# Optimization experiments

Measured on AMD Instinct MI355X. Metric: run time of the kernel, lower is better.

## Reference

```python
import jax, jax.numpy as jnp
import numpy as np

# Contiguous token segment lengths per group (static, sums to 4096)
LEN_GROUPS = (256, 512, 768, 384, 640, 512, 576, 448)
NUM_GROUPS, D_IN, D_OUT = 8, 512, 512
BATCH = 16


def setup_inputs() -> dict:
    key = jax.random.key(0)
    k1, k2, k3 = jax.random.split(key, 3)
    T = int(sum(LEN_GROUPS))
    x = jax.random.normal(k1, (BATCH, T, D_IN), dtype=jnp.float32)
    # nn.Linear default init: U(-1/sqrt(fan_in), 1/sqrt(fan_in))
    bound = 1.0 / np.sqrt(D_IN)
    W = jax.random.uniform(k2, (NUM_GROUPS, D_OUT, D_IN), jnp.float32, -bound, bound)
    b = jax.random.uniform(k3, (NUM_GROUPS, D_OUT), jnp.float32, -bound, bound)
    return {"x": x, "W": W, "b": b}


def reference(x, W, b):
    # Per-group Linear over contiguous token segments, then concat along tokens.
    # Loop is over a small static group count; segment bounds are Python ints,
    # so slicing is static and jit-compatible.
    outs = []
    start = 0
    for i, L in enumerate(LEN_GROUPS):
        seg = x[:, start:start + L]                     # [B, L, D_in]
        outs.append(jnp.einsum('btd,od->bto', seg, W[i]) + b[i])  # [B, L, D_out]
        start += L
    return jnp.concatenate(outs, axis=1)               # [B, T, D_out]
```

## Files before the change

### kernel.cpp

```cpp
#include <hip/hip_runtime.h>
#include <hip/hip_bf16.h>
#include <cstdint>

#define BATCH 16
#define TTOT  4096
#define DIN   512
#define DOUT  512
#define NG    8
#define NJOB  33

typedef float f32x4 __attribute__((ext_vector_type(4)));
typedef short s16x8 __attribute__((ext_vector_type(8)));

__device__ __forceinline__ short f2b(float f) {
    union { __bf16 b; short s; } u; u.b = (__bf16)f; return u.s;
}

__device__ __constant__ short JT0[NJOB] = {
    0,128, 256,384,512,640, 768,896,1024,1152,1280,1408, 1536,1664,1792,
    1920,2048,2176,2304,2432, 2560,2688,2816,2944, 3072,3200,3328,3456,
    3584, 3648, 3712,3840,3968};
__device__ __constant__ char JG[NJOB] = {
    0,0, 1,1,1,1, 2,2,2,2,2,2, 3,3,3, 4,4,4,4,4, 5,5,5,5, 6,6,6,6, 6, 7, 7,7,7};
__device__ __constant__ char JNW[NJOB] = {
    8,8, 8,8,8,8, 8,8,8,8,8,8, 8,8,8, 8,8,8,8,8, 8,8,8,8, 8,8,8,8, 4, 4, 8,8,8};

__global__ void wconv_kernel(const float* __restrict__ W, ushort* __restrict__ wbf) {
    int gid = blockIdx.x * 256 + threadIdx.x;
    int c = gid >> 10;
    int q = (gid & 1023) << 4;
    int row = q >> 7;
    int bc  = q & 127;
    int kbyte = bc ^ ((row & 7) << 4);
    int kt = c & 7, nt = (c >> 3) & 3, g = c >> 5;
    const float* wp = W + ((size_t)(g * DOUT + nt * 128 + row)) * DIN
                        + kt * 64 + (kbyte >> 1);
    float4 v0 = *reinterpret_cast<const float4*>(wp);
    float4 v1 = *reinterpret_cast<const float4*>(wp + 4);
    s16x8 o;
    o[0]=f2b(v0.x); o[1]=f2b(v0.y); o[2]=f2b(v0.z); o[3]=f2b(v0.w);
    o[4]=f2b(v1.x); o[5]=f2b(v1.y); o[6]=f2b(v1.z); o[7]=f2b(v1.w);
    *reinterpret_cast<s16x8*>((char*)wbf + (size_t)c * 16384 + q) = o;
}

__launch_bounds__(512, 2)
__global__ void gemm_kernel(const float* __restrict__ x,
                            const ushort* __restrict__ wbf,
                            const float* __restrict__ bias,
                            float* __restrict__ out) {
    __shared__ __align__(16) char smem[147968];
    char* ldsB = smem;
    const int tid  = threadIdx.x;
    const int lane = tid & 63;
    const int wv   = tid >> 6;
    const int colf = lane & 15;
    const int kg   = lane >> 4;
    float* cslice = (float*)(smem + 131072 + wv * 2112);

    const int p  = blockIdx.x;
    const int l  = ((p & 7) << 5) + (p >> 3);
    const int r0   = (l < 64) ? l * 9 : 8 * l + 64;
    const int rend = r0 + ((l < 64) ? 9 : 8);

    float4 st0[4], st1[4], st2[4], st3[4];

#define ISSUE(S, P, KT_) do {                                               \
        const float* p_ = (P) + ((KT_) << 6) + (kg << 3);                   \
        st##S[0] = *(const float4*)(p_);                                    \
        st##S[1] = *(const float4*)(p_ + 4);                                \
        st##S[2] = *(const float4*)(p_ + 32);                               \
        st##S[3] = *(const float4*)(p_ + 36);                               \
    } while (0)

#define CONSUME(S, KT_) do {                                                \
        _Pragma("unroll")                                                   \
        for (int ks = 0; ks < 2; ++ks) {                                    \
            float4 f0 = st##S[ks*2], f1 = st##S[ks*2+1];                    \
            s16x8 af;                                                       \
            af[0]=f2b(f0.x); af[1]=f2b(f0.y); af[2]=f2b(f0.z); af[3]=f2b(f0.w); \
            af[4]=f2b(f1.x); af[5]=f2b(f1.y); af[6]=f2b(f1.z); af[7]=f2b(f1.w); \
            const int kb = ks * 64 + (kg << 4);                             \
            _Pragma("unroll")                                               \
            for (int ni = 0; ni < 8; ++ni) {                                \
                int rb = ni * 16 + colf;                                    \
                s16x8 bf = *(const s16x8*)(ldsB + (KT_) * 16384 + (rb << 7) \
                                           + (kb ^ ((rb & 7) << 4)));       \
                acc[ni] = __builtin_amdgcn_mfma_f32_16x16x32_bf16(          \
                    af, bf, acc[ni], 0, 0, 0);                              \
            }                                                               \
        }                                                                   \
    } while (0)

#define FENCE asm volatile("" ::: "memory")

    auto abase = [&](int r) -> const float* {
        int job = r >> 6, bb = r & 15;
        return x + ((size_t)(bb * TTOT + (int)JT0[job] + (wv << 4) + colf)) * DIN;
    };

    const float* pcur = abase(r0);
    ISSUE(0, pcur, 0); ISSUE(1, pcur, 1); ISSUE(2, pcur, 2);

    int key_cur = -1;
#pragma unroll 1
    for (int r = r0; r < rend; ++r) {
        const int job = r >> 6, nt = (r >> 4) & 3, bb = r & 15;
        const int t0 = JT0[job], g = JG[job], nw = JNW[job];
        const int key = (g << 2) | nt;
        if (key != key_cur) {
            key_cur = key;
            FENCE;
            __builtin_amdgcn_s_barrier();
            FENCE;
            const char* wsrc = (const char*)wbf + (size_t)key * 131072;
#pragma unroll
            for (int i = 0; i < 16; ++i) {
                __builtin_amdgcn_global_load_lds(
                    (const __attribute__((address_space(1))) void*)(wsrc + i * 8192 + tid * 16),
                    (__attribute__((address_space(3))) void*)(ldsB + i * 8192 + tid * 16),
                    16, 0, 0);
            }
            FENCE;
            asm volatile("s_waitcnt vmcnt(0)" ::: "memory");
            __builtin_amdgcn_s_barrier();
            FENCE;
        }
        const bool hn = (r + 1 < rend);
        const float* pnext = hn ? abase(r + 1) : pcur;

        f32x4 acc[8];
#pragma unroll
        for (int ni = 0; ni < 8; ++ni) acc[ni] = (f32x4){0.f, 0.f, 0.f, 0.f};

        ISSUE(3, pcur, 3);            CONSUME(0, 0);
        ISSUE(0, pcur, 4);            CONSUME(1, 1);
        ISSUE(1, pcur, 5);            CONSUME(2, 2);
        ISSUE(2, pcur, 6);            CONSUME(3, 3);
        ISSUE(3, pcur, 7);            CONSUME(0, 4);
        if (hn) { ISSUE(0, pnext, 0); } CONSUME(1, 5);
        if (hn) { ISSUE(1, pnext, 1); } CONSUME(2, 6);
        if (hn) { ISSUE(2, pnext, 2); } CONSUME(3, 7);

        if (wv < nw) {
            const int n0 = nt << 7;
            const float4 b0 = *(const float4*)(bias + (g << 9) + n0 + (colf << 2));
            const float4 b1 = *(const float4*)(bias + (g << 9) + n0 + (colf << 2) + 64);
            const size_t orow0 = (size_t)bb * TTOT + t0 + (wv << 4);
#pragma unroll
            for (int j = 0; j < 4; ++j) {
#pragma unroll
                for (int ni = 0; ni < 8; ++ni)
                    cslice[kg * 132 + ni * 16 + colf] = acc[ni][j];
                float4 v0 = *(const float4*)(cslice + kg * 132 + (colf << 2));
                float4 v1 = *(const float4*)(cslice + kg * 132 + (colf << 2) + 64);
                float4 o0, o1;
                o0.x = v0.x + b0.x; o0.y = v0.y + b0.y;
                o0.z = v0.z + b0.z; o0.w = v0.w + b0.w;
                o1.x = v1.x + b1.x; o1.y = v1.y + b1.y;
                o1.z = v1.z + b1.z; o1.w = v1.w + b1.w;
                float* orow = out + (orow0 + (kg << 2) + j) * DOUT + n0;
                *(float4*)(orow + (colf << 2))      = o0;
                *(float4*)(orow + (colf << 2) + 64) = o1;
            }
        }
        pcur = pnext;
    }
#undef ISSUE
#undef CONSUME
#undef FENCE
}

__launch_bounds__(256)
__global__ void gemm_fallback(const float* __restrict__ x,
                              const float* __restrict__ W,
                              const float* __restrict__ bias,
                              float* __restrict__ out) {
    __shared__ __align__(16) char smem[49152];
    const int tid  = threadIdx.x;
    const int lane = tid & 63;
    const int wid  = tid >> 6;
    const int wm   = wid >> 1;
    const int wn   = wid & 1;
    const int p  = blockIdx.x;
    const int l  = ((p & 7) << 9) + (p >> 3);
    const int mt = l >> 2;
    const int nt = l & 3;
    const int bb = mt >> 6;
    const int t0 = (mt & 63) << 6;
    const int n0 = nt << 7;
    int g = 0;
    if (t0 >= 256)  g++; if (t0 >= 768)  g++; if (t0 >= 1536) g++;
    if (t0 >= 1920) g++; if (t0 >= 2560) g++; if (t0 >= 3072) g++;
    if (t0 >= 3648) g++;
    const int arow = tid >> 2;
    const int acol = (tid & 3) << 4;
    const float* aptr = x + ((size_t)(bb * TTOT + t0 + arow)) * DIN + acol;
    float4 a0, a1, a2, a3;
    float4 bw0[4], bw1[4];
    auto load_global = [&](int k0) {
        a0 = *(const float4*)(aptr + k0);
        a1 = *(const float4*)(aptr + k0 + 4);
        a2 = *(const float4*)(aptr + k0 + 8);
        a3 = *(const float4*)(aptr + k0 + 12);
#pragma unroll
        for (int pp = 0; pp < 4; ++pp) {
            int idx = pp * 256 + tid;
            int row = idx >> 3, seg = idx & 7;
            const float* wp = W + ((size_t)((g << 9) + n0 + row)) * DIN + k0 + (seg << 3);
            bw0[pp] = *(const float4*)(wp);
            bw1[pp] = *(const float4*)(wp + 4);
        }
    };
    auto swz = [](int row, int bc) { return (row << 7) + (bc ^ ((row & 7) << 4)); };
    auto write_lds = [&](int buf) {
        char* ab  = smem + buf * 8192;
        char* bb_ = smem + 16384 + buf * 16384;
        s16x8 w0, w1;
        w0[0]=f2b(a0.x); w0[1]=f2b(a0.y); w0[2]=f2b(a0.z); w0[3]=f2b(a0.w);
        w0[4]=f2b(a1.x); w0[5]=f2b(a1.y); w0[6]=f2b(a1.z); w0[7]=f2b(a1.w);
        w1[0]=f2b(a2.x); w1[1]=f2b(a2.y); w1[2]=f2b(a2.z); w1[3]=f2b(a2.w);
        w1[4]=f2b(a3.x); w1[5]=f2b(a3.y); w1[6]=f2b(a3.z); w1[7]=f2b(a3.w);
        const int abase2 = acol << 1;
        *(s16x8*)(ab + swz(arow, abase2))      = w0;
        *(s16x8*)(ab + swz(arow, abase2 + 16)) = w1;
#pragma unroll
        for (int pp = 0; pp < 4; ++pp) {
            int idx = pp * 256 + tid;
            int row = idx >> 3, seg = idx & 7;
            s16x8 wvv;
            wvv[0]=f2b(bw0[pp].x); wvv[1]=f2b(bw0[pp].y);
            wvv[2]=f2b(bw0[pp].z); wvv[3]=f2b(bw0[pp].w);
            wvv[4]=f2b(bw1[pp].x); wvv[5]=f2b(bw1[pp].y);
            wvv[6]=f2b(bw1[pp].z); wvv[7]=f2b(bw1[pp].w);
            *(s16x8*)(bb_ + swz(row, seg << 4)) = wvv;
        }
    };
    f32x4 acc[2][4];
#pragma unroll
    for (int mi = 0; mi < 2; ++mi)
#pragma unroll
        for (int ni = 0; ni < 4; ++ni) acc[mi][ni] = (f32x4){0.f,0.f,0.f,0.f};
    const int colf = lane & 15;
    const int kgrp = lane >> 4;
    auto compute = [&](int buf) {
        const char* ab  = smem + buf * 8192;
        const char* bb_ = smem + 16384 + buf * 16384;
#pragma unroll
        for (int ks = 0; ks < 2; ++ks) {
            const int kb = ks * 64 + kgrp * 16;
            s16x8 af[2], bf[4];
#pragma unroll
            for (int mi = 0; mi < 2; ++mi)
                af[mi] = *(const s16x8*)(ab + swz(wm * 32 + mi * 16 + colf, kb));
#pragma unroll
            for (int ni = 0; ni < 4; ++ni)
                bf[ni] = *(const s16x8*)(bb_ + swz(wn * 64 + ni * 16 + colf, kb));
#pragma unroll
            for (int mi = 0; mi < 2; ++mi)
#pragma unroll
                for (int ni = 0; ni < 4; ++ni)
                    acc[mi][ni] = __builtin_amdgcn_mfma_f32_16x16x32_bf16(
                        af[mi], bf[ni], acc[mi][ni], 0, 0, 0);
        }
    };
    load_global(0);
    write_lds(0);
    __syncthreads();
    int buf = 0;
#pragma unroll 1
    for (int kt = 0; kt < 8; ++kt) {
        if (kt < 7) load_global((kt + 1) << 6);
        compute(buf);
        if (kt < 7) write_lds(buf ^ 1);
        __syncthreads();
        buf ^= 1;
    }
    float* cbuf = (float*)smem;
#pragma unroll
    for (int ni = 0; ni < 4; ++ni) {
        const int c = wn * 64 + ni * 16 + colf;
#pragma unroll
        for (int mi = 0; mi < 2; ++mi) {
            const int r = wm * 32 + mi * 16 + kgrp * 4;
            f32x4 v = acc[mi][ni];
            cbuf[(r + 0) * 132 + c] = v[0];
            cbuf[(r + 1) * 132 + c] = v[1];
            cbuf[(r + 2) * 132 + c] = v[2];
            cbuf[(r + 3) * 132 + c] = v[3];
        }
    }
    __syncthreads();
    const int rr = tid >> 5;
    const int cc = (tid & 31) << 2;
    const float4 bv = *(const float4*)(bias + (g << 9) + n0 + cc);
#pragma unroll
    for (int it = 0; it < 8; ++it) {
        const int row = it * 8 + rr;
        float4 v = *(const float4*)(cbuf + row * 132 + cc);
        float4 o4; o4.x = v.x + bv.x; o4.y = v.y + bv.y;
                   o4.z = v.z + bv.z; o4.w = v.w + bv.w;
        *(float4*)(out + ((size_t)(bb * TTOT) + t0 + row) * DOUT + n0 + cc) = o4;
    }
}

extern "C" void kernel_launch(void* const* d_in, const int* in_sizes, int n_in,
                              void* d_out, int out_size, void* d_ws, size_t ws_size,
                              hipStream_t stream) {
    const float* x    = (const float*)d_in[0];
    const float* W    = (const float*)d_in[1];
    const float* bias = (const float*)d_in[2];
    float* out = (float*)d_out;

    const size_t wbytes = (size_t)NG * DOUT * DIN * sizeof(ushort);

    if (ws_size >= wbytes) {
        ushort* wbf = (ushort*)d_ws;
        wconv_kernel<<<1024, 256, 0, stream>>>(W, wbf);
        gemm_kernel<<<256, 512, 0, stream>>>(x, wbf, bias, out);
    } else {
        gemm_fallback<<<BATCH * 64 * 4, 256, 0, stream>>>(x, W, bias, out);
    }
}
```

Baseline: 105.7 us.

## Restructure grouped GEMM into 64-column N-chunks with flattened batch-token tiles

The GEMM is redone so each block owns one 64-column output chunk of one group, keeping a 64 KB bf16 weight slice resident in LDS that is loaded once. Each block walks flattened (batch, token) rows, using magic-number division to map them back to batch and token. This replaces the per-job weight reloads and barriers, as well as the LDS-staged output transpose. The grid doubles to 512 blocks with occupancy 4, and the rows are register-prefetched two k-steps ahead. A risk is that x rows are now re-read eight times across N-chunks (versus four before), and output stores become scalar instead of float4.

```diff
diff --git a/kernel.cpp b/kernel.cpp
--- a/kernel.cpp
+++ b/kernel.cpp
@@ -7,7 +7,6 @@
 #define DIN   512
 #define DOUT  512
 #define NG    8
-#define NJOB  33
 
 typedef float f32x4 __attribute__((ext_vector_type(4)));
 typedef short s16x8 __attribute__((ext_vector_type(8)));
@@ -16,158 +15,177 @@
     union { __bf16 b; short s; } u; u.b = (__bf16)f; return u.s;
 }
 
-__device__ __constant__ short JT0[NJOB] = {
-    0,128, 256,384,512,640, 768,896,1024,1152,1280,1408, 1536,1664,1792,
-    1920,2048,2176,2304,2432, 2560,2688,2816,2944, 3072,3200,3328,3456,
-    3584, 3648, 3712,3840,3968};
-__device__ __constant__ char JG[NJOB] = {
-    0,0, 1,1,1,1, 2,2,2,2,2,2, 3,3,3, 4,4,4,4,4, 5,5,5,5, 6,6,6,6, 6, 7, 7,7,7};
-__device__ __constant__ char JNW[NJOB] = {
-    8,8, 8,8,8,8, 8,8,8,8,8,8, 8,8,8, 8,8,8,8,8, 8,8,8,8, 8,8,8,8, 4, 4, 8,8,8};
+__device__ __constant__ short GT0[8] = {0,256,768,1536,1920,2560,3072,3648};
+__device__ __constant__ short GL[8]  = {256,512,768,384,640,512,576,448};
+__device__ __constant__ int   GM[8]  = {16385,8193,5462,10923,6554,8193,7282,9363};
+__device__ __constant__ char PG[64] = {
+    0,0,0,0,
+    1,1,1,1,1,1,1,1,
+    2,2,2,2,2,2,2,2,2,2,2,2,
+    3,3,3,3,3,3,
+    4,4,4,4,4,4,4,4,4,4,
+    5,5,5,5,5,5,5,5,
+    6,6,6,6,6,6,6,6,6,
+    7,7,7,7,7,7,7};
+__device__ __constant__ char PS[64] = {
+    0,1,2,3,
+    0,1,2,3,4,5,6,7,
+    0,1,2,3,4,5,6,7,8,9,10,11,
+    0,1,2,3,4,5,
+    0,1,2,3,4,5,6,7,8,9,
+    0,1,2,3,4,5,6,7,
+    0,1,2,3,4,5,6,7,8,
+    0,1,2,3,4,5,6};
 
 __global__ void wconv_kernel(const float* __restrict__ W, ushort* __restrict__ wbf) {
     int gid = blockIdx.x * 256 + threadIdx.x;
-    int c = gid >> 10;
-    int q = (gid & 1023) << 4;
+    int c = gid >> 9;
+    int q = (gid & 511) << 4;
     int row = q >> 7;
     int bc  = q & 127;
     int kbyte = bc ^ ((row & 7) << 4);
-    int kt = c & 7, nt = (c >> 3) & 3, g = c >> 5;
-    const float* wp = W + ((size_t)(g * DOUT + nt * 128 + row)) * DIN
-                        + kt * 64 + (kbyte >> 1);
+    int kt = c & 7, nc = (c >> 3) & 7, g = c >> 6;
+    const float* wp = W + ((size_t)((g << 9) + (nc << 6) + row) << 9)
+                        + (kt << 6) + (kbyte >> 1);
     float4 v0 = *reinterpret_cast<const float4*>(wp);
     float4 v1 = *reinterpret_cast<const float4*>(wp + 4);
     s16x8 o;
     o[0]=f2b(v0.x); o[1]=f2b(v0.y); o[2]=f2b(v0.z); o[3]=f2b(v0.w);
     o[4]=f2b(v1.x); o[5]=f2b(v1.y); o[6]=f2b(v1.z); o[7]=f2b(v1.w);
-    *reinterpret_cast<s16x8*>((char*)wbf + (size_t)c * 16384 + q) = o;
-}
-
-__launch_bounds__(512, 2)
+    *reinterpret_cast<s16x8*>((char*)wbf + (size_t)c * 8192 + q) = o;
+}
+
+__launch_bounds__(512, 4)
 __global__ void gemm_kernel(const float* __restrict__ x,
                             const ushort* __restrict__ wbf,
                             const float* __restrict__ bias,
                             float* __restrict__ out) {
-    __shared__ __align__(16) char smem[147968];
-    char* ldsB = smem;
+    __shared__ __align__(16) char ldsB[65536];
+
     const int tid  = threadIdx.x;
     const int lane = tid & 63;
     const int wv   = tid >> 6;
     const int colf = lane & 15;
     const int kg   = lane >> 4;
-    float* cslice = (float*)(smem + 131072 + wv * 2112);
-
-    const int p  = blockIdx.x;
-    const int l  = ((p & 7) << 5) + (p >> 3);
-    const int r0   = (l < 64) ? l * 9 : 8 * l + 64;
-    const int rend = r0 + ((l < 64) ? 9 : 8);
-
-    float4 st0[4], st1[4], st2[4], st3[4];
-
-#define ISSUE(S, P, KT_) do {                                               \
-        const float* p_ = (P) + ((KT_) << 6) + (kg << 3);                   \
-        st##S[0] = *(const float4*)(p_);                                    \
-        st##S[1] = *(const float4*)(p_ + 4);                                \
-        st##S[2] = *(const float4*)(p_ + 32);                               \
-        st##S[3] = *(const float4*)(p_ + 36);                               \
+
+    const int p    = blockIdx.x;
+    const int nc   = (p >> 3) & 7;
+    const int pair = (p & 7) + ((p >> 6) << 3);
+    const int g    = PG[pair];
+    const int s    = PS[pair];
+    const int t0g  = GT0[g];
+    const int Lg   = GL[g];
+    const int Mg   = GM[g];
+
+    const char* wsrc = (const char*)wbf + (size_t)((g << 3) + nc) * 65536;
+#pragma unroll
+    for (int i = 0; i < 8; ++i)
+        __builtin_amdgcn_global_load_lds(
+            (const __attribute__((address_space(1))) void*)(wsrc + i * 8192 + tid * 16),
+            (__attribute__((address_space(3))) void*)(ldsB + i * 8192 + tid * 16),
+            16, 0, 0);
+    asm volatile("s_waitcnt vmcnt(0)" ::: "memory");
+    __builtin_amdgcn_s_barrier();
+
+    float bv[4];
+#pragma unroll
+    for (int ni = 0; ni < 4; ++ni)
+        bv[ni] = bias[(g << 9) + (nc << 6) + (ni << 4) + colf];
+
+    const int swz = (colf & 7) << 4;
+    int bcoA[4], bcoB[4];
+#pragma unroll
+    for (int ni = 0; ni < 4; ++ni) {
+        int base = (((ni << 4) + colf) << 7) + ((kg << 4) ^ swz);
+        bcoA[ni] = base;
+        bcoB[ni] = base ^ 64;
+    }
+
+    const int fbase = s << 10;
+
+    auto aptr = [&](int f) -> const float* {
+        int bb = ((f >> 6) * Mg) >> 16;
+        int tt = f - bb * Lg;
+        return x + ((size_t)((bb << 12) + t0g + tt) << 9) + (kg << 3);
+    };
+
+    float4 sA[2][2][2];
+    const float *a0, *a1, *na0, *na1;
+
+#define LD(SL, KS) do {                                        \
+        sA[SL][0][0] = *(const float4*)(a0 + (KS) * 32);       \
+        sA[SL][0][1] = *(const float4*)(a0 + (KS) * 32 + 4);   \
+        sA[SL][1][0] = *(const float4*)(a1 + (KS) * 32);       \
+        sA[SL][1][1] = *(const float4*)(a1 + (KS) * 32 + 4);   \
     } while (0)
 
-#define CONSUME(S, KT_) do {                                                \
-        _Pragma("unroll")                                                   \
-        for (int ks = 0; ks < 2; ++ks) {                                    \
-            float4 f0 = st##S[ks*2], f1 = st##S[ks*2+1];                    \
-            s16x8 af;                                                       \
-            af[0]=f2b(f0.x); af[1]=f2b(f0.y); af[2]=f2b(f0.z); af[3]=f2b(f0.w); \
-            af[4]=f2b(f1.x); af[5]=f2b(f1.y); af[6]=f2b(f1.z); af[7]=f2b(f1.w); \
-            const int kb = ks * 64 + (kg << 4);                             \
-            _Pragma("unroll")                                               \
-            for (int ni = 0; ni < 8; ++ni) {                                \
-                int rb = ni * 16 + colf;                                    \
-                s16x8 bf = *(const s16x8*)(ldsB + (KT_) * 16384 + (rb << 7) \
-                                           + (kb ^ ((rb & 7) << 4)));       \
-                acc[ni] = __builtin_amdgcn_mfma_f32_16x16x32_bf16(          \
-                    af, bf, acc[ni], 0, 0, 0);                              \
-            }                                                               \
-        }                                                                   \
-    } while (0)
-
-#define FENCE asm volatile("" ::: "memory")
-
-    auto abase = [&](int r) -> const float* {
-        int job = r >> 6, bb = r & 15;
-        return x + ((size_t)(bb * TTOT + (int)JT0[job] + (wv << 4) + colf)) * DIN;
-    };
-
-    const float* pcur = abase(r0);
-    ISSUE(0, pcur, 0); ISSUE(1, pcur, 1); ISSUE(2, pcur, 2);
-
-    int key_cur = -1;
+    {
+        int f0 = fbase + (wv << 5);
+        a0 = aptr(f0 + colf);
+        a1 = aptr(f0 + 16 + colf);
+    }
+    LD(0, 0);
+    LD(1, 1);
+
 #pragma unroll 1
-    for (int r = r0; r < rend; ++r) {
-        const int job = r >> 6, nt = (r >> 4) & 3, bb = r & 15;
-        const int t0 = JT0[job], g = JG[job], nw = JNW[job];
-        const int key = (g << 2) | nt;
-        if (key != key_cur) {
-            key_cur = key;
-            FENCE;
-            __builtin_amdgcn_s_barrier();
-            FENCE;
-            const char* wsrc = (const char*)wbf + (size_t)key * 131072;
-#pragma unroll
-            for (int i = 0; i < 16; ++i) {
-                __builtin_amdgcn_global_load_lds(
-                    (const __attribute__((address_space(1))) void*)(wsrc + i * 8192 + tid * 16),
-                    (__attribute__((address_space(3))) void*)(ldsB + i * 8192 + tid * 16),
-                    16, 0, 0);
+    for (int t = 0; t < 4; ++t) {
+        f32x4 acc[2][4];
+#pragma unroll
+        for (int mi = 0; mi < 2; ++mi)
+#pragma unroll
+            for (int ni = 0; ni < 4; ++ni)
+                acc[mi][ni] = (f32x4){0.f, 0.f, 0.f, 0.f};
+
+#pragma unroll
+        for (int ks = 0; ks < 16; ++ks) {
+            s16x8 af[2];
+#pragma unroll
+            for (int mi = 0; mi < 2; ++mi) {
+                float4 lo = sA[ks & 1][mi][0], hi = sA[ks & 1][mi][1];
+                s16x8 o;
+                o[0]=f2b(lo.x); o[1]=f2b(lo.y); o[2]=f2b(lo.z); o[3]=f2b(lo.w);
+                o[4]=f2b(hi.x); o[5]=f2b(hi.y); o[6]=f2b(hi.z); o[7]=f2b(hi.w);
+                af[mi] = o;
             }
-            FENCE;
-            asm volatile("s_waitcnt vmcnt(0)" ::: "memory");
-            __builtin_amdgcn_s_barrier();
-            FENCE;
-        }
-        const bool hn = (r + 1 < rend);
-        const float* pnext = hn ? abase(r + 1) : pcur;
-
-        f32x4 acc[8];
-#pragma unroll
-        for (int ni = 0; ni < 8; ++ni) acc[ni] = (f32x4){0.f, 0.f, 0.f, 0.f};
-
-        ISSUE(3, pcur, 3);            CONSUME(0, 0);
-        ISSUE(0, pcur, 4);            CONSUME(1, 1);
-        ISSUE(1, pcur, 5);            CONSUME(2, 2);
-        ISSUE(2, pcur, 6);            CONSUME(3, 3);
-        ISSUE(3, pcur, 7);            CONSUME(0, 4);
-        if (hn) { ISSUE(0, pnext, 0); } CONSUME(1, 5);
-        if (hn) { ISSUE(1, pnext, 1); } CONSUME(2, 6);
-        if (hn) { ISSUE(2, pnext, 2); } CONSUME(3, 7);
-
-        if (wv < nw) {
-            const int n0 = nt << 7;
-            const float4 b0 = *(const float4*)(bias + (g << 9) + n0 + (colf << 2));
-            const float4 b1 = *(const float4*)(bias + (g << 9) + n0 + (colf << 2) + 64);
-            const size_t orow0 = (size_t)bb * TTOT + t0 + (wv << 4);
+            if (ks == 13 && t < 3) {
+                int f0n = fbase + ((((t + 1) << 3) + wv) << 5);
+                na0 = aptr(f0n + colf);
+                na1 = aptr(f0n + 16 + colf);
+            }
+            if (ks <= 13) {
+                LD(ks & 1, ks + 2);
+            } else if (t < 3) {
+                if (ks == 14) { a0 = na0; a1 = na1; LD(0, 0); }
+                else          { LD(1, 1); }
+            }
+            const char* bsl = ldsB + ((ks >> 1) << 13);
+            s16x8 bf[4];
+#pragma unroll
+            for (int ni = 0; ni < 4; ++ni)
+                bf[ni] = *(const s16x8*)(bsl + ((ks & 1) ? bcoB[ni] : bcoA[ni]));
+#pragma unroll
+            for (int mi = 0; mi < 2; ++mi)
+#pragma unroll
+                for (int ni = 0; ni < 4; ++ni)
+                    acc[mi][ni] = __builtin_amdgcn_mfma_f32_16x16x32_bf16(
+                        af[mi], bf[ni], acc[mi][ni], 0, 0, 0);
+        }
+
+        const int ftile = fbase + (((t << 3) + wv) << 5);
+#pragma unroll
+        for (int mi = 0; mi < 2; ++mi)
 #pragma unroll
             for (int j = 0; j < 4; ++j) {
-#pragma unroll
-                for (int ni = 0; ni < 8; ++ni)
-                    cslice[kg * 132 + ni * 16 + colf] = acc[ni][j];
-                float4 v0 = *(const float4*)(cslice + kg * 132 + (colf << 2));
-                float4 v1 = *(const float4*)(cslice + kg * 132 + (colf << 2) + 64);
-                float4 o0, o1;
-                o0.x = v0.x + b0.x; o0.y = v0.y + b0.y;
-                o0.z = v0.z + b0.z; o0.w = v0.w + b0.w;
-                o1.x = v1.x + b1.x; o1.y = v1.y + b1.y;
-                o1.z = v1.z + b1.z; o1.w = v1.w + b1.w;
-                float* orow = out + (orow0 + (kg << 2) + j) * DOUT + n0;
-                *(float4*)(orow + (colf << 2))      = o0;
-                *(float4*)(orow + (colf << 2) + 64) = o1;
+                int f = ftile + (mi << 4) + (kg << 2) + j;
+                int bb = ((f >> 6) * Mg) >> 16;
+                int tt = f - bb * Lg;
+                float* orow = out + ((size_t)((bb << 12) + t0g + tt) << 9) + (nc << 6);
+#pragma unroll
+                for (int ni = 0; ni < 4; ++ni)
+                    orow[(ni << 4) + colf] = acc[mi][ni][j] + bv[ni];
             }
-        }
-        pcur = pnext;
-    }
-#undef ISSUE
-#undef CONSUME
-#undef FENCE
+    }
+#undef LD
 }
 
 __launch_bounds__(256)
@@ -211,7 +229,7 @@
             bw1[pp] = *(const float4*)(wp + 4);
         }
     };
-    auto swz = [](int row, int bc) { return (row << 7) + (bc ^ ((row & 7) << 4)); };
+    auto swzf = [](int row, int bc) { return (row << 7) + (bc ^ ((row & 7) << 4)); };
     auto write_lds = [&](int buf) {
         char* ab  = smem + buf * 8192;
         char* bb_ = smem + 16384 + buf * 16384;
@@ -221,8 +239,8 @@
         w1[0]=f2b(a2.x); w1[1]=f2b(a2.y); w1[2]=f2b(a2.z); w1[3]=f2b(a2.w);
         w1[4]=f2b(a3.x); w1[5]=f2b(a3.y); w1[6]=f2b(a3.z); w1[7]=f2b(a3.w);
         const int abase2 = acol << 1;
-        *(s16x8*)(ab + swz(arow, abase2))      = w0;
-        *(s16x8*)(ab + swz(arow, abase2 + 16)) = w1;
+        *(s16x8*)(ab + swzf(arow, abase2))      = w0;
+        *(s16x8*)(ab + swzf(arow, abase2 + 16)) = w1;
 #pragma unroll
         for (int pp = 0; pp < 4; ++pp) {
             int idx = pp * 256 + tid;
@@ -232,7 +250,7 @@
             wvv[2]=f2b(bw0[pp].z); wvv[3]=f2b(bw0[pp].w);
             wvv[4]=f2b(bw1[pp].x); wvv[5]=f2b(bw1[pp].y);
             wvv[6]=f2b(bw1[pp].z); wvv[7]=f2b(bw1[pp].w);
-            *(s16x8*)(bb_ + swz(row, seg << 4)) = wvv;
+            *(s16x8*)(bb_ + swzf(row, seg << 4)) = wvv;
         }
     };
     f32x4 acc[2][4];
@@ -251,10 +269,10 @@
             s16x8 af[2], bf[4];
 #pragma unroll
             for (int mi = 0; mi < 2; ++mi)
-                af[mi] = *(const s16x8*)(ab + swz(wm * 32 + mi * 16 + colf, kb));
+                af[mi] = *(const s16x8*)(ab + swzf(wm * 32 + mi * 16 + colf, kb));
 #pragma unroll
             for (int ni = 0; ni < 4; ++ni)
-                bf[ni] = *(const s16x8*)(bb_ + swz(wn * 64 + ni * 16 + colf, kb));
+                bf[ni] = *(const s16x8*)(bb_ + swzf(wn * 64 + ni * 16 + colf, kb));
 #pragma unroll
             for (int mi = 0; mi < 2; ++mi)
 #pragma unroll
@@ -292,13 +310,13 @@
     __syncthreads();
     const int rr = tid >> 5;
     const int cc = (tid & 31) << 2;
-    const float4 bv = *(const float4*)(bias + (g << 9) + n0 + cc);
+    const float4 bvv = *(const float4*)(bias + (g << 9) + n0 + cc);
 #pragma unroll
     for (int it = 0; it < 8; ++it) {
         const int row = it * 8 + rr;
         float4 v = *(const float4*)(cbuf + row * 132 + cc);
-        float4 o4; o4.x = v.x + bv.x; o4.y = v.y + bv.y;
-                   o4.z = v.z + bv.z; o4.w = v.w + bv.w;
+        float4 o4; o4.x = v.x + bvv.x; o4.y = v.y + bvv.y;
+                   o4.z = v.z + bvv.z; o4.w = v.w + bvv.w;
         *(float4*)(out + ((size_t)(bb * TTOT) + t0 + row) * DOUT + n0 + cc) = o4;
     }
 }
@@ -316,7 +334,7 @@
     if (ws_size >= wbytes) {
         ushort* wbf = (ushort*)d_ws;
         wconv_kernel<<<1024, 256, 0, stream>>>(W, wbf);
-        gemm_kernel<<<256, 512, 0, stream>>>(x, wbf, bias, out);
+        gemm_kernel<<<512, 512, 0, stream>>>(x, wbf, bias, out);
     } else {
         gemm_fallback<<<BATCH * 64 * 4, 256, 0, stream>>>(x, W, bias, out);
     }
```

Result: slower. 335.6 us (+217.7%).
